# Kernel optimization log

Measured on AMD Instinct MI355X. Metric: run time of the kernel, lower is better.

## Reference

```python
import jax, jax.numpy as jnp
import numpy as np

B, S, D, H, FF, L, V, NC = 16, 512, 768, 12, 3072, 6, 30522, 3
HD = D // H

def _ln(x, s, b, eps=1e-12):
    m = jnp.mean(x, axis=-1, keepdims=True)
    v = jnp.var(x, axis=-1, keepdims=True)
    return (x - m) * jax.lax.rsqrt(v + eps) * s + b

def setup_inputs():
    key = jax.random.key(0)
    ks = jax.random.split(key, 16)
    p = lambda k, shape: jax.random.normal(k, shape, jnp.float32) * 0.02
    return {
        'input_ids': jax.random.randint(ks[0], (B, S), 0, V, dtype=jnp.int32),
        'segment_ids': jnp.sort(jax.random.randint(ks[1], (B, S), 0, S, dtype=jnp.int32), axis=-1),
        'attention_mask': jnp.ones((B, S), jnp.int32),
        'label_ids': jax.random.randint(ks[2], (B,), 0, NC, dtype=jnp.int32),
        'emb_table': p(ks[3], (V, D)),
        'pos_emb': p(ks[4], (S, D)),
        'emb_ln_s': jnp.ones((D,)), 'emb_ln_b': jnp.zeros((D,)),
        'Wq': p(ks[5], (L, D, D)), 'bq': jnp.zeros((L, D)),
        'Wk': p(ks[6], (L, D, D)), 'bk': jnp.zeros((L, D)),
        'Wv': p(ks[7], (L, D, D)), 'bv': jnp.zeros((L, D)),
        'Wo': p(ks[8], (L, D, D)), 'bo': jnp.zeros((L, D)),
        'ln1_s': jnp.ones((L, D)), 'ln1_b': jnp.zeros((L, D)),
        'W1': p(ks[9], (L, D, FF)), 'b1': jnp.zeros((L, FF)),
        'W2': p(ks[10], (L, FF, D)), 'b2': jnp.zeros((L, D)),
        'ln2_s': jnp.ones((L, D)), 'ln2_b': jnp.zeros((L, D)),
        'pre_W': p(ks[11], (D, D)), 'pre_b': jnp.zeros((D,)),
        'cls_W': p(ks[12], (D, NC)), 'cls_b': jnp.zeros((NC,)),
    }

def reference(input_ids, segment_ids, attention_mask, label_ids, emb_table, pos_emb,
              emb_ln_s, emb_ln_b, Wq, bq, Wk, bk, Wv, bv, Wo, bo, ln1_s, ln1_b,
              W1, b1, W2, b2, ln2_s, ln2_b, pre_W, pre_b, cls_W, cls_b):
    # --- ragged sub-token merge: vectorized segment-sum replacing the python loops ---
    embeds = emb_table[input_ids]                                   # [B,S,D]
    seg = jax.vmap(lambda e, s: jax.ops.segment_sum(e, s, num_segments=S))(embeds, segment_ids)
    cnt = jax.vmap(lambda s: jax.ops.segment_sum(jnp.ones((S,), embeds.dtype), s, num_segments=S))(segment_ids)
    pad_emb = emb_table[0]                                          # emb of token id 0, as in original
    merged = jnp.where(cnt[..., None] > 0, seg, pad_emb)            # [B,S,D]
    # --- DistilBERT encoder ---
    x = _ln(merged + pos_emb[None], emb_ln_s, emb_ln_b)
    mask_bias = jnp.where(attention_mask[:, None, None, :] == 0, -1e9, 0.0).astype(x.dtype)

    def layer(x, prm):
        wq, bq_, wk, bk_, wv, bv_, wo, bo_, l1s, l1b, w1, b1_, w2, b2_, l2s, l2b = prm
        q = (x @ wq + bq_).reshape(B, S, H, HD)
        k = (x @ wk + bk_).reshape(B, S, H, HD)
        v = (x @ wv + bv_).reshape(B, S, H, HD)
        scores = jnp.einsum('bqhd,bkhd->bhqk', q, k) / np.float32(np.sqrt(HD)) + mask_bias
        a = jax.nn.softmax(scores, axis=-1)
        ctx = jnp.einsum('bhqk,bkhd->bqhd', a, v).reshape(B, S, D)
        x = _ln(x + ctx @ wo + bo_, l1s, l1b)
        h = jax.nn.gelu(x @ w1 + b1_, approximate=False)
        x = _ln(x + h @ w2 + b2_, l2s, l2b)
        return x, None

    prms = (Wq, bq, Wk, bk, Wv, bv, Wo, bo, ln1_s, ln1_b, W1, b1, W2, b2, ln2_s, ln2_b)
    x, _ = jax.lax.scan(layer, x, prms)
    # --- classification head ---
    cls = jax.nn.relu(x[:, 0] @ pre_W + pre_b)
    logits = cls @ cls_W + cls_b                                    # [B, NC]
    return logits
```

## Files before the change

kernel.cpp:

```cpp
#include <hip/hip_runtime.h>

typedef __bf16 bf16_t;
typedef __bf16 bf16x8 __attribute__((ext_vector_type(8)));
typedef float f32x4 __attribute__((ext_vector_type(4)));

#define NB 16
#define NS 512
#define ND 768
#define NH 12
#define NFF 3072
#define NL 6
#define NHD 64
#define NM (NB*NS)

static __device__ __forceinline__ f32x4 mfma16(bf16x8 a, bf16x8 b, f32x4 c) {
    return __builtin_amdgcn_mfma_f32_16x16x32_bf16(a, b, c, 0, 0, 0);
}

static __device__ __forceinline__ float loadf(const void* p, size_t i, int isbf) {
    return isbf ? (float)((const bf16_t*)p)[i] : ((const float*)p)[i];
}

__global__ void detect_dtype(const void* elns, int* flag) {
    if (threadIdx.x == 0 && blockIdx.x == 0) {
        unsigned u = *(const unsigned*)elns;
        *flag = (u != 0x3F800000u) ? 1 : 0;
    }
}

__global__ __launch_bounds__(256) void transpose_bt(const void* __restrict__ src, size_t eoff,
                                                    bf16_t* __restrict__ dst, int K, int N,
                                                    const int* __restrict__ flagp) {
    const int isbf = flagp[0];
    __shared__ bf16_t t[32][33];
    int nn0 = blockIdx.x * 32, kk0 = blockIdx.y * 32;
    int tx = threadIdx.x, ty = threadIdx.y;
    #pragma unroll
    for (int i = 0; i < 4; i++)
        t[ty + i*8][tx] = (bf16_t)loadf(src, eoff + (size_t)(kk0 + ty + i*8) * N + nn0 + tx, isbf);
    __syncthreads();
    #pragma unroll
    for (int i = 0; i < 4; i++)
        dst[(size_t)(nn0 + ty + i*8) * K + kk0 + tx] = t[tx][ty + i*8];
}

static __device__ __forceinline__ void blockReduce2(float& a, float& b, float* redbuf, int tid) {
    #pragma unroll
    for (int o = 32; o; o >>= 1) { a += __shfl_xor(a, o); b += __shfl_xor(b, o); }
    int wv = tid >> 6;
    if ((tid & 63) == 0) { redbuf[wv] = a; redbuf[4 + wv] = b; }
    __syncthreads();
    a = redbuf[0] + redbuf[1] + redbuf[2] + redbuf[3];
    b = redbuf[4] + redbuf[5] + redbuf[6] + redbuf[7];
    __syncthreads();
}

__global__ __launch_bounds__(256) void embed_ln(const int* __restrict__ ids,
                                                const int* __restrict__ segs,
                                                const void* __restrict__ emb,
                                                const void* __restrict__ pos,
                                                const void* __restrict__ gamma,
                                                const void* __restrict__ beta,
                                                float* __restrict__ x, bf16_t* __restrict__ xb,
                                                const int* __restrict__ flagp) {
    const int isbf = flagp[0];
    int b = blockIdx.y, sq = blockIdx.x, tid = threadIdx.x;
    __shared__ int slo, shi;
    __shared__ float redbuf[8];
    if (tid == 0) { slo = 1 << 30; shi = -1; }
    __syncthreads();
    const int* segrow = segs + b * NS;
    const int* idrow  = ids  + b * NS;
    for (int p = tid; p < NS; p += 256)
        if (segrow[p] == sq) { atomicMin(&slo, p); atomicMax(&shi, p); }
    __syncthreads();
    int lo = slo, hi = shi;
    float vals[3];
    #pragma unroll
    for (int i = 0; i < 3; i++) {
        int d = tid + i * 256;
        float s;
        if (hi >= lo) {
            s = 0.f;
            for (int p = lo; p <= hi; p++) s += loadf(emb, (size_t)idrow[p] * ND + d, isbf);
        } else {
            s = loadf(emb, d, isbf);
        }
        vals[i] = s + loadf(pos, (size_t)sq * ND + d, isbf);
    }
    float sum = vals[0] + vals[1] + vals[2];
    float sq2 = vals[0]*vals[0] + vals[1]*vals[1] + vals[2]*vals[2];
    blockReduce2(sum, sq2, redbuf, tid);
    float mean = sum / ND;
    float var  = sq2 / ND - mean * mean;
    float rs = rsqrtf(fmaxf(var, 0.f) + 1e-12f);
    size_t rowoff = ((size_t)b * NS + sq) * ND;
    #pragma unroll
    for (int i = 0; i < 3; i++) {
        int d = tid + i * 256;
        float o = (vals[i] - mean) * rs * loadf(gamma, d, isbf) + loadf(beta, d, isbf);
        x[rowoff + d] = o;
        xb[rowoff + d] = (bf16_t)o;
    }
}

__global__ __launch_bounds__(256) void ln_rows(float* __restrict__ x,
                                               const void* __restrict__ gamma, size_t goff,
                                               const void* __restrict__ beta, size_t boff,
                                               bf16_t* __restrict__ xb,
                                               const int* __restrict__ flagp) {
    const int isbf = flagp[0];
    int row = blockIdx.x, tid = threadIdx.x;
    __shared__ float redbuf[8];
    size_t rowoff = (size_t)row * ND;
    float vals[3];
    #pragma unroll
    for (int i = 0; i < 3; i++) vals[i] = x[rowoff + tid + i * 256];
    float sum = vals[0] + vals[1] + vals[2];
    float sq2 = vals[0]*vals[0] + vals[1]*vals[1] + vals[2]*vals[2];
    blockReduce2(sum, sq2, redbuf, tid);
    float mean = sum / ND;
    float var  = sq2 / ND - mean * mean;
    float rs = rsqrtf(fmaxf(var, 0.f) + 1e-12f);
    #pragma unroll
    for (int i = 0; i < 3; i++) {
        int d = tid + i * 256;
        float o = (vals[i] - mean) * rs * loadf(gamma, goff + d, isbf) + loadf(beta, boff + d, isbf);
        x[rowoff + d] = o;
        xb[rowoff + d] = (bf16_t)o;
    }
}

__global__ __launch_bounds__(256) void gemm_bt(const bf16_t* __restrict__ A,
                                               const bf16_t* __restrict__ Bt,
                                               const void* __restrict__ bias, size_t boff,
                                               void* __restrict__ out,
                                               int N_, int K_, int mode,
                                               const int* __restrict__ flagp) {
    const int isbf = flagp[0];
    __shared__ __align__(16) bf16_t As[128][72];
    __shared__ __align__(16) bf16_t Bs[128][72];
    int tid = threadIdx.x, wave = tid >> 6, lane = tid & 63;
    int lm = lane & 15, quad = lane >> 4;
    int m0 = blockIdx.y * 128, n0 = blockIdx.x * 128;
    int wm = (wave >> 1) * 64, wn = (wave & 1) * 64;
    f32x4 acc[4][4] = {};
    const bf16_t* Arow = A + (size_t)m0 * K_;
    const bf16_t* Brow = Bt + (size_t)n0 * K_;
    int ra = tid >> 3, ca = (tid & 7) * 8;
    for (int k0 = 0; k0 < K_; k0 += 64) {
        __syncthreads();
        #pragma unroll
        for (int i = 0; i < 4; i++) {
            int r = ra + i * 32;
            *(bf16x8*)(&As[r][ca]) = *(const bf16x8*)(Arow + (size_t)r * K_ + k0 + ca);
            *(bf16x8*)(&Bs[r][ca]) = *(const bf16x8*)(Brow + (size_t)r * K_ + k0 + ca);
        }
        __syncthreads();
        #pragma unroll
        for (int ks = 0; ks < 64; ks += 32) {
            bf16x8 af[4], bfv[4];
            #pragma unroll
            for (int t = 0; t < 4; t++) {
                af[t]  = *(const bf16x8*)(&As[wm + t*16 + lm][ks + quad*8]);
                bfv[t] = *(const bf16x8*)(&Bs[wn + t*16 + lm][ks + quad*8]);
            }
            #pragma unroll
            for (int mt = 0; mt < 4; mt++)
                #pragma unroll
                for (int nt = 0; nt < 4; nt++)
                    acc[mt][nt] = mfma16(af[mt], bfv[nt], acc[mt][nt]);
        }
    }
    #pragma unroll
    for (int mt = 0; mt < 4; mt++)
    #pragma unroll
    for (int nt = 0; nt < 4; nt++)
    #pragma unroll
    for (int r = 0; r < 4; r++) {
        int mrow = m0 + wm + mt*16 + quad*4 + r;
        int ncol = n0 + wn + nt*16 + lm;
        float val = acc[mt][nt][r] + loadf(bias, boff + ncol, isbf);
        if (mode == 0) {
            int bb = mrow >> 9, sp = mrow & 511, hh = ncol >> 6, hd = ncol & 63;
            ((bf16_t*)out)[(((size_t)(bb*NH + hh) * NS) + sp) * NHD + hd] = (bf16_t)val;
        } else if (mode == 1) {
            size_t idx = (size_t)mrow * N_ + ncol;
            ((float*)out)[idx] += val;
        } else {
            size_t idx = (size_t)mrow * N_ + ncol;
            float g = 0.5f * val * (1.0f + erff(val * 0.70710678118654752f));
            ((bf16_t*)out)[idx] = (bf16_t)g;
        }
    }
}

__global__ __launch_bounds__(256) void attn(const bf16_t* __restrict__ q,
                                            const bf16_t* __restrict__ k,
                                            const bf16_t* __restrict__ v,
                                            const int* __restrict__ mask,
                                            bf16_t* __restrict__ ctx) {
    __shared__ __align__(16) bf16_t sc[32][520];
    __shared__ __align__(16) bf16_t kv[64][72];
    __shared__ float rinv[32];
    int tid = threadIdx.x, w = tid >> 6, lane = tid & 63;
    int lm = lane & 15, quad = lane >> 4;
    int mtw = w >> 1, nhw = w & 1;
    int b = blockIdx.z, h = blockIdx.y, q0 = blockIdx.x * 32;
    const bf16_t* Qg = q + (((size_t)(b*NH + h) * NS) + q0) * NHD;
    const bf16_t* Kg = k + ((size_t)(b*NH + h) * NS) * NHD;
    const bf16_t* Vg = v + ((size_t)(b*NH + h) * NS) * NHD;
    bf16x8 aq0 = *(const bf16x8*)(Qg + (mtw*16 + lm) * NHD + quad*8);
    bf16x8 aq1 = *(const bf16x8*)(Qg + (mtw*16 + lm) * NHD + 32 + quad*8);
    int sr = tid >> 2, scol = (tid & 3) * 16;
    for (int kc = 0; kc < NS; kc += 64) {
        __syncthreads();
        *(bf16x8*)(&kv[sr][scol])     = *(const bf16x8*)(Kg + (size_t)(kc + sr) * NHD + scol);
        *(bf16x8*)(&kv[sr][scol + 8]) = *(const bf16x8*)(Kg + (size_t)(kc + sr) * NHD + scol + 8);
        __syncthreads();
        #pragma unroll
        for (int nt = 0; nt < 2; nt++) {
            int ncl = nhw*32 + nt*16 + lm;
            bf16x8 b0 = *(const bf16x8*)(&kv[ncl][quad*8]);
            bf16x8 b1 = *(const bf16x8*)(&kv[ncl][32 + quad*8]);
            f32x4 a = {};
            a = mfma16(aq0, b0, a);
            a = mfma16(aq1, b1, a);
            int col = kc + ncl;
            float mb = (mask[b*NS + col] == 0) ? -1e9f : 0.0f;
            #pragma unroll
            for (int r = 0; r < 4; r++)
                sc[mtw*16 + quad*4 + r][col] = (bf16_t)(a[r] * 0.125f + mb);
        }
    }
    __syncthreads();
    for (int r = 0; r < 8; r++) {
        int row = w*8 + r;
        float mx = -3.0e38f;
        #pragma unroll
        for (int i = 0; i < 8; i++) mx = fmaxf(mx, (float)sc[row][lane + i*64]);
        #pragma unroll
        for (int o = 32; o; o >>= 1) mx = fmaxf(mx, __shfl_xor(mx, o));
        float sum = 0.f;
        #pragma unroll
        for (int i = 0; i < 8; i++) {
            float p = __expf((float)sc[row][lane + i*64] - mx);
            sc[row][lane + i*64] = (bf16_t)p;
            sum += p;
        }
        #pragma unroll
        for (int o = 32; o; o >>= 1) sum += __shfl_xor(sum, o);
        if (lane == 0) rinv[row] = 1.0f / sum;
    }
    f32x4 oc[2] = {};
    for (int kc = 0; kc < NS; kc += 64) {
        __syncthreads();
        {
            bf16x8 v0 = *(const bf16x8*)(Vg + (size_t)(kc + sr) * NHD + scol);
            bf16x8 v1 = *(const bf16x8*)(Vg + (size_t)(kc + sr) * NHD + scol + 8);
            #pragma unroll
            for (int j = 0; j < 8; j++) { kv[scol + j][sr] = v0[j]; kv[scol + 8 + j][sr] = v1[j]; }
        }
        __syncthreads();
        #pragma unroll
        for (int ks = 0; ks < 2; ks++) {
            bf16x8 ap = *(const bf16x8*)(&sc[mtw*16 + lm][kc + ks*32 + quad*8]);
            #pragma unroll
            for (int nt = 0; nt < 2; nt++) {
                int d = nhw*32 + nt*16 + lm;
                bf16x8 bv = *(const bf16x8*)(&kv[d][ks*32 + quad*8]);
                oc[nt] = mfma16(ap, bv, oc[nt]);
            }
        }
    }
    #pragma unroll
    for (int nt = 0; nt < 2; nt++)
    #pragma unroll
    for (int r = 0; r < 4; r++) {
        int row = mtw*16 + quad*4 + r;
        float val = oc[nt][r] * rinv[row];
        ctx[((size_t)(b*NS) + q0 + row) * ND + h*NHD + nhw*32 + nt*16 + lm] = (bf16_t)val;
    }
}

__global__ __launch_bounds__(256) void head(const float* __restrict__ x,
                                            const void* __restrict__ preW,
                                            const void* __restrict__ preb,
                                            const void* __restrict__ clsW,
                                            const void* __restrict__ clsb,
                                            void* __restrict__ out,
                                            const int* __restrict__ flagp) {
    const int isbf = flagp[0];
    int b = blockIdx.x, tid = threadIdx.x;
    __shared__ float xr[ND];
    __shared__ float pr[ND];
    __shared__ float red[256];
    for (int d = tid; d < ND; d += 256) xr[d] = x[((size_t)b * NS) * ND + d];
    __syncthreads();
    for (int n = tid; n < ND; n += 256) {
        float s = loadf(preb, n, isbf);
        for (int kk = 0; kk < ND; kk++) s += xr[kk] * loadf(preW, (size_t)kk * ND + n, isbf);
        pr[n] = fmaxf(s, 0.f);
    }
    __syncthreads();
    for (int c = 0; c < 3; c++) {
        float s = 0.f;
        for (int kk = tid; kk < ND; kk += 256) s += pr[kk] * loadf(clsW, kk * 3 + c, isbf);
        red[tid] = s;
        __syncthreads();
        for (int off = 128; off; off >>= 1) {
            if (tid < off) red[tid] += red[tid + off];
            __syncthreads();
        }
        if (tid == 0) {
            float v = red[0] + loadf(clsb, c, isbf);
            if (isbf) ((bf16_t*)out)[b * 3 + c] = (bf16_t)v;
            else      ((float*)out)[b * 3 + c] = v;
        }
        __syncthreads();
    }
}

static const size_t SZ_ACT_BF = (size_t)NM * ND * 2;
static const size_t SZ_ACT_F  = (size_t)NM * ND * 4;
static const size_t SZ_WSQ    = (size_t)ND * ND * 2;
static const size_t SZ_WF     = (size_t)ND * NFF * 2;
static const size_t OFF_QB   = 0;
static const size_t OFF_KB   = OFF_QB + SZ_ACT_BF;
static const size_t OFF_VB   = OFF_KB + SZ_ACT_BF;
static const size_t OFF_CTX  = OFF_VB + SZ_ACT_BF;
static const size_t OFF_X    = OFF_CTX + SZ_ACT_BF;
static const size_t OFF_XB   = OFF_X + SZ_ACT_F;
static const size_t OFF_WQ   = OFF_XB + SZ_ACT_BF;
static const size_t OFF_WK   = OFF_WQ + SZ_WSQ;
static const size_t OFF_WV   = OFF_WK + SZ_WSQ;
static const size_t OFF_WO   = OFF_WV + SZ_WSQ;
static const size_t OFF_W1   = OFF_WO + SZ_WSQ;
static const size_t OFF_W2   = OFF_W1 + SZ_WF;
static const size_t OFF_FLAG = OFF_W2 + SZ_WF;

extern "C" void kernel_launch(void* const* d_in, const int* in_sizes, int n_in,
                              void* d_out, int out_size, void* d_ws, size_t ws_size,
                              hipStream_t stream) {
    const int* ids   = (const int*)d_in[0];
    const int* segs  = (const int*)d_in[1];
    const int* mask  = (const int*)d_in[2];
    const void* emb  = d_in[4];
    const void* pos  = d_in[5];
    const void* elns = d_in[6];
    const void* elnb = d_in[7];
    const void* Wq = d_in[8];  const void* bq = d_in[9];
    const void* Wk = d_in[10]; const void* bk = d_in[11];
    const void* Wv = d_in[12]; const void* bv = d_in[13];
    const void* Wo = d_in[14]; const void* bo = d_in[15];
    const void* l1s = d_in[16]; const void* l1b = d_in[17];
    const void* W1 = d_in[18];  const void* b1 = d_in[19];
    const void* W2 = d_in[20];  const void* b2 = d_in[21];
    const void* l2s = d_in[22]; const void* l2b = d_in[23];
    const void* preW = d_in[24]; const void* preb = d_in[25];
    const void* clsW = d_in[26]; const void* clsb = d_in[27];

    char* ws = (char*)d_ws;
    bf16_t* qb   = (bf16_t*)(ws + OFF_QB);
    bf16_t* kb   = (bf16_t*)(ws + OFF_KB);
    bf16_t* vb   = (bf16_t*)(ws + OFF_VB);
    bf16_t* ctxb = (bf16_t*)(ws + OFF_CTX);
    bf16_t* h1b  = (bf16_t*)(ws + OFF_QB);
    float*  x    = (float*)(ws + OFF_X);
    bf16_t* xb   = (bf16_t*)(ws + OFF_XB);
    bf16_t* wq_t = (bf16_t*)(ws + OFF_WQ);
    bf16_t* wk_t = (bf16_t*)(ws + OFF_WK);
    bf16_t* wv_t = (bf16_t*)(ws + OFF_WV);
    bf16_t* wo_t = (bf16_t*)(ws + OFF_WO);
    bf16_t* w1_t = (bf16_t*)(ws + OFF_W1);
    bf16_t* w2_t = (bf16_t*)(ws + OFF_W2);
    int*    flag = (int*)(ws + OFF_FLAG);

    detect_dtype<<<1, 64, 0, stream>>>(elns, flag);
    embed_ln<<<dim3(NS, NB), 256, 0, stream>>>(ids, segs, emb, pos, elns, elnb, x, xb, flag);

    dim3 tb(32, 8);
    for (int l = 0; l < NL; l++) {
        size_t oq = (size_t)l * ND * ND, of = (size_t)l * ND * NFF;
        transpose_bt<<<dim3(24, 24), tb, 0, stream>>>(Wq, oq, wq_t, ND, ND, flag);
        transpose_bt<<<dim3(24, 24), tb, 0, stream>>>(Wk, oq, wk_t, ND, ND, flag);
        transpose_bt<<<dim3(24, 24), tb, 0, stream>>>(Wv, oq, wv_t, ND, ND, flag);
        transpose_bt<<<dim3(24, 24), tb, 0, stream>>>(Wo, oq, wo_t, ND, ND, flag);
        transpose_bt<<<dim3(96, 24), tb, 0, stream>>>(W1, of, w1_t, ND, NFF, flag);
        transpose_bt<<<dim3(24, 96), tb, 0, stream>>>(W2, of, w2_t, NFF, ND, flag);

        gemm_bt<<<dim3(6, 64), 256, 0, stream>>>(xb, wq_t, bq, (size_t)l*ND, qb, ND, ND, 0, flag);
        gemm_bt<<<dim3(6, 64), 256, 0, stream>>>(xb, wk_t, bk, (size_t)l*ND, kb, ND, ND, 0, flag);
        gemm_bt<<<dim3(6, 64), 256, 0, stream>>>(xb, wv_t, bv, (size_t)l*ND, vb, ND, ND, 0, flag);
        attn<<<dim3(16, NH, NB), 256, 0, stream>>>(qb, kb, vb, mask, ctxb);
        gemm_bt<<<dim3(6, 64), 256, 0, stream>>>(ctxb, wo_t, bo, (size_t)l*ND, x, ND, ND, 1, flag);
        ln_rows<<<NM, 256, 0, stream>>>(x, l1s, (size_t)l*ND, l1b, (size_t)l*ND, xb, flag);
        gemm_bt<<<dim3(24, 64), 256, 0, stream>>>(xb, w1_t, b1, (size_t)l*NFF, h1b, NFF, ND, 2, flag);
        gemm_bt<<<dim3(6, 64), 256, 0, stream>>>(h1b, w2_t, b2, (size_t)l*ND, x, ND, NFF, 1, flag);
        ln_rows<<<NM, 256, 0, stream>>>(x, l2s, (size_t)l*ND, l2b, (size_t)l*ND, xb, flag);
    }

    head<<<NB, 256, 0, stream>>>(x, preW, preb, clsW, clsb, d_out, flag);
}
```

Measured before the change: 3.557 ms.

## Fuse QKV GEMM, use direct-to-LDS swizzled loads, batch weight transposes, vectorize softmax

```diff
diff --git a/kernel.cpp b/kernel.cpp
--- a/kernel.cpp
+++ b/kernel.cpp
@@ -12,6 +12,7 @@
 #define NL 6
 #define NHD 64
 #define NM (NB*NS)
+static const size_t NQKV = (size_t)NB * NH * NS * NHD;
 
 static __device__ __forceinline__ f32x4 mfma16(bf16x8 a, bf16x8 b, f32x4 c) {
     return __builtin_amdgcn_mfma_f32_16x16x32_bf16(a, b, c, 0, 0, 0);
@@ -19,6 +20,11 @@
 
 static __device__ __forceinline__ float loadf(const void* p, size_t i, int isbf) {
     return isbf ? (float)((const bf16_t*)p)[i] : ((const float*)p)[i];
+}
+
+static __device__ __forceinline__ void gload_lds16(const bf16_t* g, bf16_t* l) {
+    __builtin_amdgcn_global_load_lds((const __attribute__((address_space(1))) void*)g,
+                                     (__attribute__((address_space(3))) void*)l, 16, 0, 0);
 }
 
 __global__ void detect_dtype(const void* elns, int* flag) {
@@ -28,20 +34,24 @@
     }
 }
 
-__global__ __launch_bounds__(256) void transpose_bt(const void* __restrict__ src, size_t eoff,
-                                                    bf16_t* __restrict__ dst, int K, int N,
-                                                    const int* __restrict__ flagp) {
+__global__ __launch_bounds__(256) void transpose_bt(const void* __restrict__ src, size_t src_off,
+                                                    size_t src_lstride,
+                                                    bf16_t* __restrict__ dst, size_t dst_lstride,
+                                                    int K, int N, const int* __restrict__ flagp) {
     const int isbf = flagp[0];
     __shared__ bf16_t t[32][33];
+    int l = blockIdx.z;
+    size_t so = src_off + (size_t)l * src_lstride;
+    bf16_t* d = dst + (size_t)l * dst_lstride;
     int nn0 = blockIdx.x * 32, kk0 = blockIdx.y * 32;
     int tx = threadIdx.x, ty = threadIdx.y;
     #pragma unroll
     for (int i = 0; i < 4; i++)
-        t[ty + i*8][tx] = (bf16_t)loadf(src, eoff + (size_t)(kk0 + ty + i*8) * N + nn0 + tx, isbf);
+        t[ty + i*8][tx] = (bf16_t)loadf(src, so + (size_t)(kk0 + ty + i*8) * N + nn0 + tx, isbf);
     __syncthreads();
     #pragma unroll
     for (int i = 0; i < 4; i++)
-        dst[(size_t)(nn0 + ty + i*8) * K + kk0 + tx] = t[tx][ty + i*8];
+        d[(size_t)(nn0 + ty + i*8) * K + kk0 + tx] = t[tx][ty + i*8];
 }
 
 static __device__ __forceinline__ void blockReduce2(float& a, float& b, float* redbuf, int tid) {
@@ -133,37 +143,43 @@
 
 __global__ __launch_bounds__(256) void gemm_bt(const bf16_t* __restrict__ A,
                                                const bf16_t* __restrict__ Bt,
-                                               const void* __restrict__ bias, size_t boff,
-                                               void* __restrict__ out,
+                                               const void* __restrict__ bias0,
+                                               const void* __restrict__ bias1,
+                                               const void* __restrict__ bias2,
+                                               size_t boff, void* __restrict__ out,
                                                int N_, int K_, int mode,
                                                const int* __restrict__ flagp) {
     const int isbf = flagp[0];
-    __shared__ __align__(16) bf16_t As[128][72];
-    __shared__ __align__(16) bf16_t Bs[128][72];
+    __shared__ __align__(16) bf16_t As[128 * 64];
+    __shared__ __align__(16) bf16_t Bs[128 * 64];
     int tid = threadIdx.x, wave = tid >> 6, lane = tid & 63;
     int lm = lane & 15, quad = lane >> 4;
     int m0 = blockIdx.y * 128, n0 = blockIdx.x * 128;
     int wm = (wave >> 1) * 64, wn = (wave & 1) * 64;
     f32x4 acc[4][4] = {};
-    const bf16_t* Arow = A + (size_t)m0 * K_;
-    const bf16_t* Brow = Bt + (size_t)n0 * K_;
-    int ra = tid >> 3, ca = (tid & 7) * 8;
+    const bf16_t* Ag = A + (size_t)m0 * K_;
+    const bf16_t* Bg = Bt + (size_t)n0 * K_;
+    int lr = lane >> 3, lc = lane & 7;
     for (int k0 = 0; k0 < K_; k0 += 64) {
         __syncthreads();
         #pragma unroll
-        for (int i = 0; i < 4; i++) {
-            int r = ra + i * 32;
-            *(bf16x8*)(&As[r][ca]) = *(const bf16x8*)(Arow + (size_t)r * K_ + k0 + ca);
-            *(bf16x8*)(&Bs[r][ca]) = *(const bf16x8*)(Brow + (size_t)r * K_ + k0 + ca);
-        }
-        __syncthreads();
-        #pragma unroll
-        for (int ks = 0; ks < 64; ks += 32) {
+        for (int j = 0; j < 4; j++) {
+            int sg = wave * 4 + j;
+            int r  = sg * 8 + lr;
+            int c  = lc ^ (r & 7);
+            gload_lds16(Ag + (size_t)r * K_ + k0 + c * 8, As + sg * 512);
+            gload_lds16(Bg + (size_t)r * K_ + k0 + c * 8, Bs + sg * 512);
+        }
+        __syncthreads();
+        #pragma unroll
+        for (int ks = 0; ks < 2; ks++) {
             bf16x8 af[4], bfv[4];
             #pragma unroll
             for (int t = 0; t < 4; t++) {
-                af[t]  = *(const bf16x8*)(&As[wm + t*16 + lm][ks + quad*8]);
-                bfv[t] = *(const bf16x8*)(&Bs[wn + t*16 + lm][ks + quad*8]);
+                int ra = wm + t*16 + lm;
+                af[t]  = *(const bf16x8*)(As + ra*64 + (((ks*4 + quad) ^ (ra & 7)) << 3));
+                int rb = wn + t*16 + lm;
+                bfv[t] = *(const bf16x8*)(Bs + rb*64 + (((ks*4 + quad) ^ (rb & 7)) << 3));
             }
             #pragma unroll
             for (int mt = 0; mt < 4; mt++)
@@ -180,14 +196,19 @@
     for (int r = 0; r < 4; r++) {
         int mrow = m0 + wm + mt*16 + quad*4 + r;
         int ncol = n0 + wn + nt*16 + lm;
-        float val = acc[mt][nt][r] + loadf(bias, boff + ncol, isbf);
         if (mode == 0) {
-            int bb = mrow >> 9, sp = mrow & 511, hh = ncol >> 6, hd = ncol & 63;
-            ((bf16_t*)out)[(((size_t)(bb*NH + hh) * NS) + sp) * NHD + hd] = (bf16_t)val;
+            int which = ncol / 768;
+            int col = ncol - which * 768;
+            const void* bsel = which == 0 ? bias0 : (which == 1 ? bias1 : bias2);
+            float val = acc[mt][nt][r] + loadf(bsel, boff + col, isbf);
+            int bbx = mrow >> 9, sp = mrow & 511, hh = col >> 6, hd = col & 63;
+            ((bf16_t*)out)[(size_t)which * NQKV + (((size_t)(bbx*NH + hh) * NS) + sp) * NHD + hd] = (bf16_t)val;
         } else if (mode == 1) {
+            float val = acc[mt][nt][r] + loadf(bias0, boff + ncol, isbf);
             size_t idx = (size_t)mrow * N_ + ncol;
             ((float*)out)[idx] += val;
         } else {
+            float val = acc[mt][nt][r] + loadf(bias0, boff + ncol, isbf);
             size_t idx = (size_t)mrow * N_ + ncol;
             float g = 0.5f * val * (1.0f + erff(val * 0.70710678118654752f));
             ((bf16_t*)out)[idx] = (bf16_t)g;
@@ -234,23 +255,36 @@
         }
     }
     __syncthreads();
-    for (int r = 0; r < 8; r++) {
-        int row = w*8 + r;
+    {
+        int row = tid >> 3, part = tid & 7;
+        bf16_t* base = &sc[row][part * 64];
+        bf16x8 pv[8];
         float mx = -3.0e38f;
         #pragma unroll
-        for (int i = 0; i < 8; i++) mx = fmaxf(mx, (float)sc[row][lane + i*64]);
-        #pragma unroll
-        for (int o = 32; o; o >>= 1) mx = fmaxf(mx, __shfl_xor(mx, o));
+        for (int i = 0; i < 8; i++) {
+            pv[i] = *(const bf16x8*)(base + i * 8);
+            #pragma unroll
+            for (int j = 0; j < 8; j++) mx = fmaxf(mx, (float)pv[i][j]);
+        }
+        mx = fmaxf(mx, __shfl_xor(mx, 1));
+        mx = fmaxf(mx, __shfl_xor(mx, 2));
+        mx = fmaxf(mx, __shfl_xor(mx, 4));
         float sum = 0.f;
         #pragma unroll
         for (int i = 0; i < 8; i++) {
-            float p = __expf((float)sc[row][lane + i*64] - mx);
-            sc[row][lane + i*64] = (bf16_t)p;
-            sum += p;
-        }
-        #pragma unroll
-        for (int o = 32; o; o >>= 1) sum += __shfl_xor(sum, o);
-        if (lane == 0) rinv[row] = 1.0f / sum;
+            bf16x8 pe;
+            #pragma unroll
+            for (int j = 0; j < 8; j++) {
+                float p = __expf((float)pv[i][j] - mx);
+                pe[j] = (bf16_t)p;
+                sum += p;
+            }
+            *(bf16x8*)(base + i * 8) = pe;
+        }
+        sum += __shfl_xor(sum, 1);
+        sum += __shfl_xor(sum, 2);
+        sum += __shfl_xor(sum, 4);
+        if (part == 0) rinv[row] = 1.0f / sum;
     }
     f32x4 oc[2] = {};
     for (int kc = 0; kc < NS; kc += 64) {
@@ -283,29 +317,32 @@
     }
 }
 
-__global__ __launch_bounds__(256) void head(const float* __restrict__ x,
-                                            const void* __restrict__ preW,
-                                            const void* __restrict__ preb,
-                                            const void* __restrict__ clsW,
-                                            const void* __restrict__ clsb,
-                                            void* __restrict__ out,
-                                            const int* __restrict__ flagp) {
+__global__ __launch_bounds__(256) void head_pre(const float* __restrict__ x,
+                                                const void* __restrict__ preW,
+                                                const void* __restrict__ preb,
+                                                float* __restrict__ pr,
+                                                const int* __restrict__ flagp) {
+    const int isbf = flagp[0];
+    int b = blockIdx.y;
+    int n = blockIdx.x * 256 + threadIdx.x;
+    const float* xr = x + (size_t)b * NS * ND;
+    float s = loadf(preb, n, isbf);
+    #pragma unroll 4
+    for (int kk = 0; kk < ND; kk++) s += xr[kk] * loadf(preW, (size_t)kk * ND + n, isbf);
+    pr[b * ND + n] = fmaxf(s, 0.f);
+}
+
+__global__ __launch_bounds__(256) void head_cls(const float* __restrict__ pr,
+                                                const void* __restrict__ clsW,
+                                                const void* __restrict__ clsb,
+                                                void* __restrict__ out,
+                                                const int* __restrict__ flagp) {
     const int isbf = flagp[0];
     int b = blockIdx.x, tid = threadIdx.x;
-    __shared__ float xr[ND];
-    __shared__ float pr[ND];
     __shared__ float red[256];
-    for (int d = tid; d < ND; d += 256) xr[d] = x[((size_t)b * NS) * ND + d];
-    __syncthreads();
-    for (int n = tid; n < ND; n += 256) {
-        float s = loadf(preb, n, isbf);
-        for (int kk = 0; kk < ND; kk++) s += xr[kk] * loadf(preW, (size_t)kk * ND + n, isbf);
-        pr[n] = fmaxf(s, 0.f);
-    }
-    __syncthreads();
     for (int c = 0; c < 3; c++) {
         float s = 0.f;
-        for (int kk = tid; kk < ND; kk += 256) s += pr[kk] * loadf(clsW, kk * 3 + c, isbf);
+        for (int kk = tid; kk < ND; kk += 256) s += pr[b * ND + kk] * loadf(clsW, kk * 3 + c, isbf);
         red[tid] = s;
         __syncthreads();
         for (int off = 128; off; off >>= 1) {
@@ -320,24 +357,6 @@
         __syncthreads();
     }
 }
-
-static const size_t SZ_ACT_BF = (size_t)NM * ND * 2;
-static const size_t SZ_ACT_F  = (size_t)NM * ND * 4;
-static const size_t SZ_WSQ    = (size_t)ND * ND * 2;
-static const size_t SZ_WF     = (size_t)ND * NFF * 2;
-static const size_t OFF_QB   = 0;
-static const size_t OFF_KB   = OFF_QB + SZ_ACT_BF;
-static const size_t OFF_VB   = OFF_KB + SZ_ACT_BF;
-static const size_t OFF_CTX  = OFF_VB + SZ_ACT_BF;
-static const size_t OFF_X    = OFF_CTX + SZ_ACT_BF;
-static const size_t OFF_XB   = OFF_X + SZ_ACT_F;
-static const size_t OFF_WQ   = OFF_XB + SZ_ACT_BF;
-static const size_t OFF_WK   = OFF_WQ + SZ_WSQ;
-static const size_t OFF_WV   = OFF_WK + SZ_WSQ;
-static const size_t OFF_WO   = OFF_WV + SZ_WSQ;
-static const size_t OFF_W1   = OFF_WO + SZ_WSQ;
-static const size_t OFF_W2   = OFF_W1 + SZ_WF;
-static const size_t OFF_FLAG = OFF_W2 + SZ_WF;
 
 extern "C" void kernel_launch(void* const* d_in, const int* in_sizes, int n_in,
                               void* d_out, int out_size, void* d_ws, size_t ws_size,
@@ -360,45 +379,71 @@
     const void* preW = d_in[24]; const void* preb = d_in[25];
     const void* clsW = d_in[26]; const void* clsb = d_in[27];
 
+    const size_t SZ_QKVB = NQKV * 2;
+    size_t off = 0;
+    auto alloc = [&](size_t sz) { size_t o = off; off = (off + sz + 255) & ~(size_t)255; return o; };
+    size_t o_qkv  = alloc(3 * SZ_QKVB);
+    size_t o_ctx  = alloc(SZ_QKVB);
+    size_t o_x    = alloc((size_t)NM * ND * 4);
+    size_t o_xb   = alloc((size_t)NM * ND * 2);
+    size_t o_pr   = alloc((size_t)NB * ND * 4);
+    size_t o_flag = alloc(256);
+    size_t o_w    = off;
+    const size_t WQKV_L = (size_t)3 * ND * ND;
+    const size_t WSQ = (size_t)ND * ND, WF = (size_t)ND * NFF;
+    size_t need_big = o_w + (NL * (WQKV_L + WSQ + 2 * WF)) * 2;
+    int big = ws_size >= need_big;
+
     char* ws = (char*)d_ws;
-    bf16_t* qb   = (bf16_t*)(ws + OFF_QB);
-    bf16_t* kb   = (bf16_t*)(ws + OFF_KB);
-    bf16_t* vb   = (bf16_t*)(ws + OFF_VB);
-    bf16_t* ctxb = (bf16_t*)(ws + OFF_CTX);
-    bf16_t* h1b  = (bf16_t*)(ws + OFF_QB);
-    float*  x    = (float*)(ws + OFF_X);
-    bf16_t* xb   = (bf16_t*)(ws + OFF_XB);
-    bf16_t* wq_t = (bf16_t*)(ws + OFF_WQ);
-    bf16_t* wk_t = (bf16_t*)(ws + OFF_WK);
-    bf16_t* wv_t = (bf16_t*)(ws + OFF_WV);
-    bf16_t* wo_t = (bf16_t*)(ws + OFF_WO);
-    bf16_t* w1_t = (bf16_t*)(ws + OFF_W1);
-    bf16_t* w2_t = (bf16_t*)(ws + OFF_W2);
-    int*    flag = (int*)(ws + OFF_FLAG);
+    bf16_t* qkv  = (bf16_t*)(ws + o_qkv);
+    bf16_t* ctxb = (bf16_t*)(ws + o_ctx);
+    bf16_t* h1b  = (bf16_t*)(ws + o_qkv);
+    float*  x    = (float*)(ws + o_x);
+    bf16_t* xb   = (bf16_t*)(ws + o_xb);
+    float*  pr   = (float*)(ws + o_pr);
+    int*    flag = (int*)(ws + o_flag);
+    size_t nlw = big ? NL : 1;
+    bf16_t* wqkv = (bf16_t*)(ws + o_w);
+    bf16_t* wo_t = wqkv + nlw * WQKV_L;
+    bf16_t* w1_t = wo_t + nlw * WSQ;
+    bf16_t* w2_t = w1_t + nlw * WF;
 
     detect_dtype<<<1, 64, 0, stream>>>(elns, flag);
     embed_ln<<<dim3(NS, NB), 256, 0, stream>>>(ids, segs, emb, pos, elns, elnb, x, xb, flag);
 
     dim3 tb(32, 8);
+    if (big) {
+        transpose_bt<<<dim3(24, 24, NL), tb, 0, stream>>>(Wq, 0, WSQ, wqkv,            WQKV_L, ND, ND, flag);
+        transpose_bt<<<dim3(24, 24, NL), tb, 0, stream>>>(Wk, 0, WSQ, wqkv + WSQ,      WQKV_L, ND, ND, flag);
+        transpose_bt<<<dim3(24, 24, NL), tb, 0, stream>>>(Wv, 0, WSQ, wqkv + 2 * WSQ,  WQKV_L, ND, ND, flag);
+        transpose_bt<<<dim3(24, 24, NL), tb, 0, stream>>>(Wo, 0, WSQ, wo_t, WSQ, ND, ND, flag);
+        transpose_bt<<<dim3(96, 24, NL), tb, 0, stream>>>(W1, 0, WF, w1_t, WF, ND, NFF, flag);
+        transpose_bt<<<dim3(24, 96, NL), tb, 0, stream>>>(W2, 0, WF, w2_t, WF, NFF, ND, flag);
+    }
+
     for (int l = 0; l < NL; l++) {
-        size_t oq = (size_t)l * ND * ND, of = (size_t)l * ND * NFF;
-        transpose_bt<<<dim3(24, 24), tb, 0, stream>>>(Wq, oq, wq_t, ND, ND, flag);
-        transpose_bt<<<dim3(24, 24), tb, 0, stream>>>(Wk, oq, wk_t, ND, ND, flag);
-        transpose_bt<<<dim3(24, 24), tb, 0, stream>>>(Wv, oq, wv_t, ND, ND, flag);
-        transpose_bt<<<dim3(24, 24), tb, 0, stream>>>(Wo, oq, wo_t, ND, ND, flag);
-        transpose_bt<<<dim3(96, 24), tb, 0, stream>>>(W1, of, w1_t, ND, NFF, flag);
-        transpose_bt<<<dim3(24, 96), tb, 0, stream>>>(W2, of, w2_t, NFF, ND, flag);
-
-        gemm_bt<<<dim3(6, 64), 256, 0, stream>>>(xb, wq_t, bq, (size_t)l*ND, qb, ND, ND, 0, flag);
-        gemm_bt<<<dim3(6, 64), 256, 0, stream>>>(xb, wk_t, bk, (size_t)l*ND, kb, ND, ND, 0, flag);
-        gemm_bt<<<dim3(6, 64), 256, 0, stream>>>(xb, wv_t, bv, (size_t)l*ND, vb, ND, ND, 0, flag);
-        attn<<<dim3(16, NH, NB), 256, 0, stream>>>(qb, kb, vb, mask, ctxb);
-        gemm_bt<<<dim3(6, 64), 256, 0, stream>>>(ctxb, wo_t, bo, (size_t)l*ND, x, ND, ND, 1, flag);
-        ln_rows<<<NM, 256, 0, stream>>>(x, l1s, (size_t)l*ND, l1b, (size_t)l*ND, xb, flag);
-        gemm_bt<<<dim3(24, 64), 256, 0, stream>>>(xb, w1_t, b1, (size_t)l*NFF, h1b, NFF, ND, 2, flag);
-        gemm_bt<<<dim3(6, 64), 256, 0, stream>>>(h1b, w2_t, b2, (size_t)l*ND, x, ND, NFF, 1, flag);
-        ln_rows<<<NM, 256, 0, stream>>>(x, l2s, (size_t)l*ND, l2b, (size_t)l*ND, xb, flag);
-    }
-
-    head<<<NB, 256, 0, stream>>>(x, preW, preb, clsW, clsb, d_out, flag);
-}
+        if (!big) {
+            transpose_bt<<<dim3(24, 24, 1), tb, 0, stream>>>(Wq, (size_t)l * WSQ, 0, wqkv,           0, ND, ND, flag);
+            transpose_bt<<<dim3(24, 24, 1), tb, 0, stream>>>(Wk, (size_t)l * WSQ, 0, wqkv + WSQ,     0, ND, ND, flag);
+            transpose_bt<<<dim3(24, 24, 1), tb, 0, stream>>>(Wv, (size_t)l * WSQ, 0, wqkv + 2 * WSQ, 0, ND, ND, flag);
+            transpose_bt<<<dim3(24, 24, 1), tb, 0, stream>>>(Wo, (size_t)l * WSQ, 0, wo_t, 0, ND, ND, flag);
+            transpose_bt<<<dim3(96, 24, 1), tb, 0, stream>>>(W1, (size_t)l * WF, 0, w1_t, 0, ND, NFF, flag);
+            transpose_bt<<<dim3(24, 96, 1), tb, 0, stream>>>(W2, (size_t)l * WF, 0, w2_t, 0, NFF, ND, flag);
+        }
+        const bf16_t* wqkv_l = big ? wqkv + (size_t)l * WQKV_L : wqkv;
+        const bf16_t* wo_l   = big ? wo_t + (size_t)l * WSQ : wo_t;
+        const bf16_t* w1_l   = big ? w1_t + (size_t)l * WF : w1_t;
+        const bf16_t* w2_l   = big ? w2_t + (size_t)l * WF : w2_t;
+
+        gemm_bt<<<dim3(18, 64), 256, 0, stream>>>(xb, wqkv_l, bq, bk, bv, (size_t)l * ND, qkv, 2304, ND, 0, flag);
+        attn<<<dim3(16, NH, NB), 256, 0, stream>>>(qkv, qkv + NQKV, qkv + 2 * NQKV, mask, ctxb);
+        gemm_bt<<<dim3(6, 64), 256, 0, stream>>>(ctxb, wo_l, bo, nullptr, nullptr, (size_t)l * ND, x, ND, ND, 1, flag);
+        ln_rows<<<NM, 256, 0, stream>>>(x, l1s, (size_t)l * ND, l1b, (size_t)l * ND, xb, flag);
+        gemm_bt<<<dim3(24, 64), 256, 0, stream>>>(xb, w1_l, b1, nullptr, nullptr, (size_t)l * NFF, h1b, NFF, ND, 2, flag);
+        gemm_bt<<<dim3(6, 64), 256, 0, stream>>>(h1b, w2_l, b2, nullptr, nullptr, (size_t)l * ND, x, ND, NFF, 1, flag);
+        ln_rows<<<NM, 256, 0, stream>>>(x, l2s, (size_t)l * ND, l2b, (size_t)l * ND, xb, flag);
+    }
+
+    head_pre<<<dim3(3, NB), 256, 0, stream>>>(x, preW, preb, pr, flag);
+    head_cls<<<NB, 256, 0, stream>>>(pr, clsW, clsb, d_out, flag);
+}
```

Result: faster. 3.009 ms (-15.4%).
